# Performance work log

Hardware: AMD Instinct MI355X
Metric: run time of the kernel (lower is better)

Reference implementation:

```python
import jax, jax.numpy as jnp
import numpy as np

B, N, S, D, H = 32, 16384, 8, 64, 128  # batch, num_inputs, num_slots, slot_size(==input_size), mlp_hidden
ITERS = 3
EPS = 1e-8
LN_EPS = 1e-5


def _ln(x, g, b):
    m = jnp.mean(x, axis=-1, keepdims=True)
    v = jnp.mean((x - m) ** 2, axis=-1, keepdims=True)
    return (x - m) * jax.lax.rsqrt(v + LN_EPS) * g + b


def setup_inputs() -> dict:
    key = jax.random.key(0)
    ks = jax.random.split(key, 20)
    s = 0.02
    return {
        "x": jax.random.normal(ks[0], (B, N, D), jnp.float32),
        "slot_noise": jax.random.normal(ks[1], (B, S, D), jnp.float32),
        "slots_mu": jax.random.normal(ks[2], (1, S, D), jnp.float32),
        "slots_log_sigma": jax.random.normal(ks[3], (1, S, D), jnp.float32) * 0.1,
        "ln_in_g": jnp.ones((D,), jnp.float32), "ln_in_b": jnp.zeros((D,), jnp.float32),
        "ln_slot_g": jnp.ones((D,), jnp.float32), "ln_slot_b": jnp.zeros((D,), jnp.float32),
        "ln_mlp_g": jnp.ones((D,), jnp.float32), "ln_mlp_b": jnp.zeros((D,), jnp.float32),
        "Wq": jax.random.normal(ks[4], (D, D), jnp.float32) * s,
        "Wk": jax.random.normal(ks[5], (D, D), jnp.float32) * s,
        "Wv": jax.random.normal(ks[6], (D, D), jnp.float32) * s,
        "W_ih": jax.random.normal(ks[7], (3 * D, D), jnp.float32) * s,
        "W_hh": jax.random.normal(ks[8], (3 * D, D), jnp.float32) * s,
        "b_ih": jnp.zeros((3 * D,), jnp.float32),
        "b_hh": jnp.zeros((3 * D,), jnp.float32),
        "W1": jax.random.normal(ks[9], (H, D), jnp.float32) * s,
        "b1": jnp.zeros((H,), jnp.float32),
        "W2": jax.random.normal(ks[10], (D, H), jnp.float32) * s,
        "b2": jnp.zeros((D,), jnp.float32),
    }


def reference(x, slot_noise, slots_mu, slots_log_sigma,
              ln_in_g, ln_in_b, ln_slot_g, ln_slot_b, ln_mlp_g, ln_mlp_b,
              Wq, Wk, Wv, W_ih, W_hh, b_ih, b_hh, W1, b1, W2, b2):
    inputs = _ln(x, ln_in_g, ln_in_b)                      # [B,N,D]
    keys = inputs @ Wk.T                                   # [B,N,D]
    values = inputs @ Wv.T                                 # [B,N,D]
    slots = slots_mu + jnp.exp(slots_log_sigma) * slot_noise  # [B,S,D]
    scale = D ** (-0.5)
    for _ in range(ITERS):
        slots_prev = slots
        q = (_ln(slots, ln_slot_g, ln_slot_b) @ Wq.T) * scale   # [B,S,D]
        attn = jax.nn.softmax(jnp.einsum('bnd,bsd->bns', keys, q), axis=2) + EPS
        attn = attn / jnp.sum(attn, axis=1, keepdims=True)      # weighted mean over inputs
        updates = jnp.einsum('bns,bnd->bsd', attn, values)      # [B,S,D]
        # GRUCell(update, hidden=slots_prev), torch semantics
        gi = updates @ W_ih.T + b_ih
        gh = slots_prev @ W_hh.T + b_hh
        i_r, i_z, i_n = jnp.split(gi, 3, axis=-1)
        h_r, h_z, h_n = jnp.split(gh, 3, axis=-1)
        r = jax.nn.sigmoid(i_r + h_r)
        z = jax.nn.sigmoid(i_z + h_z)
        n = jnp.tanh(i_n + r * h_n)
        upd = (1.0 - z) * n + z * slots_prev
        # residual MLP (full_skip=False: residual around updates)
        slots = upd + jax.nn.relu(_ln(upd, ln_mlp_g, ln_mlp_b) @ W1.T + b1) @ W2.T + b2
    return slots
```

## Files before the change

### kernel.cpp

```cpp
#include <hip/hip_runtime.h>

#define BB 32
#define NN 16384

typedef __attribute__((ext_vector_type(4))) float f4;
typedef __attribute__((ext_vector_type(8))) short short8;

__device__ __forceinline__ unsigned int f2bf(float f) {
  unsigned int u = __float_as_uint(f);
  return (u + 0x7fffu + ((u >> 16) & 1u)) >> 16;
}
__device__ __forceinline__ short bfs(float f) { return (short)f2bf(f); }

__global__ void __launch_bounds__(256) prep_kernel(
    const float* __restrict__ Wq, const float* __restrict__ Wk,
    const float* __restrict__ W_ih, const float* __restrict__ Wv,
    float* __restrict__ M, float* __restrict__ Wihv)
{
  int id = blockIdx.x * 256 + threadIdx.x;
  if (id < 4096) {
    int e1 = id >> 6, e2 = id & 63;
    float acc = 0.f;
    for (int d = 0; d < 64; ++d) acc += Wq[d * 64 + e1] * Wk[d * 64 + e2];
    M[id] = acc;
  } else {
    int t = (id - 4096) >> 6, e = id & 63;
    float acc = 0.f;
    for (int k = 0; k < 64; ++k) acc += W_ih[t * 64 + k] * Wv[k * 64 + e];
    Wihv[t * 64 + e] = acc;
  }
}

__global__ void __launch_bounds__(64) init_qk_kernel(
    const float* __restrict__ noise, const float* __restrict__ mu,
    const float* __restrict__ lsig, float* __restrict__ slots,
    const float* __restrict__ gs, const float* __restrict__ bsl,
    const float* __restrict__ M, unsigned short* __restrict__ qkb)
{
  const int bsi = blockIdx.x, l = threadIdx.x;
  const int idx = bsi * 64 + l;
  __shared__ float sh[64];
  float v = mu[idx & 511] + __expf(lsig[idx & 511]) * noise[idx];
  slots[idx] = v;
  float sm = v, sq = v * v;
#pragma unroll
  for (int m = 1; m < 64; m <<= 1) { sm += __shfl_xor(sm, m); sq += __shfl_xor(sq, m); }
  float mean = sm * (1.f / 64.f);
  float var = sq * (1.f / 64.f) - mean * mean;
  sh[l] = (v - mean) * rsqrtf(var + 1e-5f) * gs[l] + bsl[l];
  float acc = 0.f;
  for (int k = 0; k < 64; ++k) acc += sh[k] * M[k * 64 + l];
  qkb[idx] = (unsigned short)f2bf(acc * 0.125f);
}

template <int MODE>
__global__ void __launch_bounds__(256) attn_kernel(
    const float* __restrict__ x, const unsigned short* __restrict__ Xin,
    const float* __restrict__ gin, const float* __restrict__ bin,
    unsigned short* __restrict__ Xout, unsigned short* __restrict__ XnT,
    const unsigned short* __restrict__ qkb,
    float* __restrict__ Wpart, float* __restrict__ cpart)
{
  constexpr int SMS = (MODE == 0) ? 16896 : 6720;
  __shared__ __align__(16) unsigned short SMEM[SMS];

  const int tid = threadIdx.x, wave = tid >> 6, lane = tid & 63;
  const int l15 = lane & 15, quad = lane >> 4;
  const int blk = blockIdx.x;
  const int b = blk >> 5;
  const int k0 = quad * 8;

  unsigned short* xt  = (MODE == 0) ? (SMEM + wave * 3584) : nullptr;
  unsigned short* Ptw = (MODE == 0) ? (SMEM + 14336 + wave * 640)
                                    : (SMEM + wave * 640);

  const unsigned short* qrow = qkb + (((b << 3) + (l15 & 7)) << 6) + k0;
  const short8 qkA0 = *(const short8*)qrow;
  const short8 qkA1 = *(const short8*)(qrow + 32);

  f4 g0a, g0b, g1a, g1b, h0a, h0b, h1a, h1b;
  if constexpr (MODE == 0) {
    g0a = *(const f4*)(gin + k0);      g0b = *(const f4*)(gin + k0 + 4);
    g1a = *(const f4*)(gin + k0 + 32); g1b = *(const f4*)(gin + k0 + 36);
    h0a = *(const f4*)(bin + k0);      h0b = *(const f4*)(bin + k0 + 4);
    h1a = *(const f4*)(bin + k0 + 32); h1b = *(const f4*)(bin + k0 + 36);
  }

  const size_t row00 = (size_t)blk * 512 + wave * 32 + l15;
  const int nt0 = ((blk & 31) << 4) + wave;

  f4 wacc[4];
#pragma unroll
  for (int t = 0; t < 4; ++t) wacc[t] = (f4){0.f, 0.f, 0.f, 0.f};
  float cac0 = 0.f, cac1 = 0.f, cac2 = 0.f, cac3 = 0.f;

  f4 cc[2][4];
  short8 aa[2][2];
  short8 cv[4];
  const unsigned short* vB =
      (MODE == 1) ? (XnT + ((((size_t)(b << 9)) + nt0) << 11) + (l15 << 5) + (quad << 3))
                  : nullptr;

  if constexpr (MODE == 0) {
    const float* xp = x + row00 * 64 + k0;
#pragma unroll
    for (int s = 0; s < 2; ++s) {
      const float* sp = xp + s * 1024;
      cc[s][0] = *(const f4*)sp;        cc[s][1] = *(const f4*)(sp + 4);
      cc[s][2] = *(const f4*)(sp + 32); cc[s][3] = *(const f4*)(sp + 36);
    }
  } else {
    const unsigned short* xb = Xin + row00 * 64 + k0;
#pragma unroll
    for (int s = 0; s < 2; ++s) {
      aa[s][0] = *(const short8*)(xb + s * 1024);
      aa[s][1] = *(const short8*)(xb + s * 1024 + 32);
    }
#pragma unroll
    for (int t = 0; t < 4; ++t)
      cv[t] = *(const short8*)(vB + (t << 9));
  }

#pragma unroll
  for (int u = 0; u < 4; ++u) {
    f4 nc[2][4];
    short8 na[2][2];
    short8 nv[4];
    if (u < 3) {
      if constexpr (MODE == 0) {
        const float* xp = x + (row00 + (size_t)(u + 1) * 128) * 64 + k0;
#pragma unroll
        for (int s = 0; s < 2; ++s) {
          const float* sp = xp + s * 1024;
          nc[s][0] = *(const f4*)sp;        nc[s][1] = *(const f4*)(sp + 4);
          nc[s][2] = *(const f4*)(sp + 32); nc[s][3] = *(const f4*)(sp + 36);
        }
      } else {
        const unsigned short* xb = Xin + (row00 + (size_t)(u + 1) * 128) * 64 + k0;
#pragma unroll
        for (int s = 0; s < 2; ++s) {
          na[s][0] = *(const short8*)(xb + s * 1024);
          na[s][1] = *(const short8*)(xb + s * 1024 + 32);
        }
#pragma unroll
        for (int t = 0; t < 4; ++t)
          nv[t] = *(const short8*)(vB + (t << 9) + ((size_t)(u + 1) << 13));
      }
    }

#pragma unroll
    for (int s = 0; s < 2; ++s) {
      short8 a0, a1;
      if constexpr (MODE == 0) {
        float sm = 0.f, sq = 0.f;
#pragma unroll
        for (int j = 0; j < 4; ++j) {
          float v0 = cc[s][0][j], v1 = cc[s][1][j], v2 = cc[s][2][j], v3 = cc[s][3][j];
          sm += v0 + v1 + v2 + v3;
          sq += v0 * v0 + v1 * v1 + v2 * v2 + v3 * v3;
        }
        sm += __shfl_xor(sm, 16); sq += __shfl_xor(sq, 16);
        sm += __shfl_xor(sm, 32); sq += __shfl_xor(sq, 32);
        const float mean = sm * (1.f / 64.f);
        const float var = sq * (1.f / 64.f) - mean * mean;
        const float rstd = rsqrtf(var + 1e-5f);
#pragma unroll
        for (int j = 0; j < 4; ++j) {
          a0[j]     = bfs((cc[s][0][j] - mean) * rstd * g0a[j] + h0a[j]);
          a0[j + 4] = bfs((cc[s][1][j] - mean) * rstd * g0b[j] + h0b[j]);
          a1[j]     = bfs((cc[s][2][j] - mean) * rstd * g1a[j] + h1a[j]);
          a1[j + 4] = bfs((cc[s][3][j] - mean) * rstd * g1b[j] + h1b[j]);
        }
        unsigned short* xo = Xout + (row00 + (size_t)u * 128 + s * 16) * 64 + k0;
        *(short8*)xo = a0;
        *(short8*)(xo + 32) = a1;
        const int nn = s * 16 + l15;
        unsigned short* xb0 = xt + (quad << 3) + nn;
#pragma unroll
        for (int jj = 0; jj < 8; ++jj) {
          xb0[(k0 + jj) * 56]      = (unsigned short)a0[jj];
          xb0[(k0 + jj + 32) * 56] = (unsigned short)a1[jj];
        }
      } else {
        a0 = aa[s][0]; a1 = aa[s][1];
      }

      f4 lg = (f4){0.f, 0.f, 0.f, 0.f};
      lg = __builtin_amdgcn_mfma_f32_16x16x32_bf16(qkA0, a0, lg, 0, 0, 0);
      lg = __builtin_amdgcn_mfma_f32_16x16x32_bf16(qkA1, a1, lg, 0, 0, 0);
      const float e0 = __expf(lg[0]), e1 = __expf(lg[1]);
      const float e2 = __expf(lg[2]), e3 = __expf(lg[3]);
      float ss = e0 + e1 + e2 + e3;
      ss += __shfl_xor(ss, 16);
      ss += __shfl_xor(ss, 32);
      const float rs = __builtin_amdgcn_rcpf(ss * 0.5f);
      const float p0 = e0 * rs, p1 = e1 * rs, p2 = e2 * rs, p3 = e3 * rs;
      cac0 += p0; cac1 += p1; cac2 += p2; cac3 += p3;
      unsigned short* pw = Ptw + (quad << 2) * 40 + s * 16 + l15;
      pw[0]   = (unsigned short)f2bf(p0);
      pw[40]  = (unsigned short)f2bf(p1);
      pw[80]  = (unsigned short)f2bf(p2);
      pw[120] = (unsigned short)f2bf(p3);
    }

    short8 pf = *(const short8*)(Ptw + l15 * 40 + quad * 8);
#pragma unroll
    for (int t = 0; t < 4; ++t) {
      short8 cvv;
      if constexpr (MODE == 0) {
        const int rr = t * 16 + l15;
        cvv = *(const short8*)(xt + rr * 56 + (((rr >> 3) & 3) << 3) + (quad << 3));
      } else {
        cvv = cv[t];
      }
      wacc[t] = __builtin_amdgcn_mfma_f32_16x16x32_bf16(pf, cvv, wacc[t], 0, 0, 0);
    }

    if constexpr (MODE == 0) {
      unsigned short* tb = XnT + ((((size_t)(b << 9)) + nt0 + (u << 2)) << 11);
#pragma unroll
      for (int pass = 0; pass < 4; ++pass) {
        const int e = (pass << 4) + (lane >> 2);
        const int no = (lane & 3) << 3;
        const short8 vv =
            *(const short8*)(xt + e * 56 + (((e >> 3) & 3) << 3) + no);
        *(short8*)(tb + (pass << 9) + ((lane >> 2) << 5) + no) = vv;
      }
    }

    if (u < 3) {
      if constexpr (MODE == 0) {
#pragma unroll
        for (int s = 0; s < 2; ++s)
#pragma unroll
          for (int j = 0; j < 4; ++j) cc[s][j] = nc[s][j];
      } else {
#pragma unroll
        for (int s = 0; s < 2; ++s) { aa[s][0] = na[s][0]; aa[s][1] = na[s][1]; }
#pragma unroll
        for (int t = 0; t < 4; ++t) cv[t] = nv[t];
      }
    }
  }

#pragma unroll
  for (int m = 1; m < 16; m <<= 1) {
    cac0 += __shfl_xor(cac0, m); cac1 += __shfl_xor(cac1, m);
    cac2 += __shfl_xor(cac2, m); cac3 += __shfl_xor(cac3, m);
  }
  float* redw;
  float* credw;
  if constexpr (MODE == 0) {
    redw  = (float*)(SMEM + wave * 3584);
    credw = (float*)(SMEM + wave * 3584 + 1024);
  } else {
    redw  = (float*)(SMEM + 2560) + wave * 512;
    credw = (float*)(SMEM + 6656) + wave * 8;
  }
  if (l15 == 0 && quad < 2) {
    credw[quad * 4 + 0] = cac0; credw[quad * 4 + 1] = cac1;
    credw[quad * 4 + 2] = cac2; credw[quad * 4 + 3] = cac3;
  }
  if (quad < 2) {
#pragma unroll
    for (int t = 0; t < 4; ++t)
#pragma unroll
      for (int r = 0; r < 4; ++r)
        redw[(quad * 4 + r) * 64 + (t << 4) + l15] = wacc[t][r];
  }
  __syncthreads();
  for (int i = tid; i < 512; i += 256) {
    float acc = 0.f;
#pragma unroll
    for (int w = 0; w < 4; ++w) {
      const float* rw = (MODE == 0) ? (const float*)(SMEM + w * 3584)
                                    : (const float*)(SMEM + 2560) + w * 512;
      acc += rw[i];
    }
    Wpart[(size_t)blk * 512 + i] = acc;
  }
  if (tid < 8) {
    float acc = 0.f;
#pragma unroll
    for (int w = 0; w < 4; ++w) {
      const float* cw = (MODE == 0) ? (const float*)(SMEM + w * 3584 + 1024)
                                    : (const float*)(SMEM + 6656) + w * 8;
      acc += cw[tid];
    }
    cpart[blk * 8 + tid] = acc;
  }
}

__global__ void __launch_bounds__(256) update_kernel(
    const float* __restrict__ Wpart, const float* __restrict__ cpart,
    const float* __restrict__ slots, float* __restrict__ out,
    const float* __restrict__ Wihv, const float* __restrict__ W_hh,
    const float* __restrict__ b_ih, const float* __restrict__ b_hh,
    const float* __restrict__ g_mlp, const float* __restrict__ b_mlp,
    const float* __restrict__ W1, const float* __restrict__ b1,
    const float* __restrict__ W2, const float* __restrict__ b2,
    const float* __restrict__ gs, const float* __restrict__ bsl,
    const float* __restrict__ M, unsigned short* __restrict__ qkb, int make_q)
{
  const int bs = blockIdx.x;
  const int b = bs >> 3, s = bs & 7;
  const int tid = threadIdx.x;
  const int l = tid & 63, cq = tid >> 6;
  __shared__ float wred[4][64];
  __shared__ float credS[4];
  __shared__ float u_sh[64], sp_sh[64], giA[192], ghA[192], uln_sh[64], h_sh[128];

  float wp = 0.f, cp2 = 0.f;
  for (int c = cq * 8; c < cq * 8 + 8; ++c) {
    wp += Wpart[(size_t)(((b << 5) + c) * 8 + s) * 64 + l];
    cp2 += cpart[((b << 5) + c) * 8 + s];
  }
  wred[cq][l] = wp;
  if (l == 0) credS[cq] = cp2;
  __syncthreads();

  float sp = 0.f;
  if (tid < 64) {
    const float cs = credS[0] + credS[1] + credS[2] + credS[3];
    const float u = (wred[0][l] + wred[1][l] + wred[2][l] + wred[3][l]) / cs;
    sp = slots[(b * 8 + s) * 64 + l];
    u_sh[l] = u; sp_sh[l] = sp;
  }
  __syncthreads();

  if (tid < 192) {
    float accI = b_ih[tid], accH = b_hh[tid];
    const float* wi = Wihv + tid * 64;
    const float* wh = W_hh + tid * 64;
    for (int k = 0; k < 64; ++k) { accI += u_sh[k] * wi[k]; accH += sp_sh[k] * wh[k]; }
    giA[tid] = accI; ghA[tid] = accH;
  }
  __syncthreads();

  float upd = 0.f;
  if (tid < 64) {
    const float rg = 1.f / (1.f + __expf(-(giA[l] + ghA[l])));
    const float zg = 1.f / (1.f + __expf(-(giA[64 + l] + ghA[64 + l])));
    const float ng = tanhf(giA[128 + l] + rg * ghA[128 + l]);
    upd = (1.f - zg) * ng + zg * sp;
    float sm = upd, sq = upd * upd;
#pragma unroll
    for (int m = 1; m < 64; m <<= 1) { sm += __shfl_xor(sm, m); sq += __shfl_xor(sq, m); }
    const float mean = sm * (1.f / 64.f);
    const float var = sq * (1.f / 64.f) - mean * mean;
    uln_sh[l] = (upd - mean) * rsqrtf(var + 1e-5f) * g_mlp[l] + b_mlp[l];
  }
  __syncthreads();

  if (tid < 128) {
    float acc = b1[tid];
    const float* w1 = W1 + tid * 64;
    for (int k = 0; k < 64; ++k) acc += uln_sh[k] * w1[k];
    h_sh[tid] = fmaxf(acc, 0.f);
  }
  __syncthreads();

  if (tid < 64) {
    float acc = b2[l];
    const float* w2 = W2 + l * 128;
    for (int k = 0; k < 128; ++k) acc += h_sh[k] * w2[k];
    const float sv = upd + acc;
    out[(b * 8 + s) * 64 + l] = sv;
    if (make_q) {
      float sm2 = sv, sq2 = sv * sv;
#pragma unroll
      for (int m = 1; m < 64; m <<= 1) { sm2 += __shfl_xor(sm2, m); sq2 += __shfl_xor(sq2, m); }
      const float mean2 = sm2 * (1.f / 64.f);
      const float var2 = sq2 * (1.f / 64.f) - mean2 * mean2;
      u_sh[l] = (sv - mean2) * rsqrtf(var2 + 1e-5f) * gs[l] + bsl[l];
      float qa = 0.f;
      for (int k = 0; k < 64; ++k) qa += u_sh[k] * M[k * 64 + l];
      qkb[(b * 8 + s) * 64 + l] = (unsigned short)f2bf(qa * 0.125f);
    }
  }
}

extern "C" void kernel_launch(void* const* d_in, const int* in_sizes, int n_in,
                              void* d_out, int out_size, void* d_ws, size_t ws_size,
                              hipStream_t stream) {
  const float* x       = (const float*)d_in[0];
  const float* noise   = (const float*)d_in[1];
  const float* mu      = (const float*)d_in[2];
  const float* lsig    = (const float*)d_in[3];
  const float* ln_in_g = (const float*)d_in[4];
  const float* ln_in_b = (const float*)d_in[5];
  const float* ln_sl_g = (const float*)d_in[6];
  const float* ln_sl_b = (const float*)d_in[7];
  const float* ln_ml_g = (const float*)d_in[8];
  const float* ln_ml_b = (const float*)d_in[9];
  const float* Wq      = (const float*)d_in[10];
  const float* Wk      = (const float*)d_in[11];
  const float* Wv      = (const float*)d_in[12];
  const float* W_ih    = (const float*)d_in[13];
  const float* W_hh    = (const float*)d_in[14];
  const float* b_ih    = (const float*)d_in[15];
  const float* b_hh    = (const float*)d_in[16];
  const float* W1      = (const float*)d_in[17];
  const float* b1      = (const float*)d_in[18];
  const float* W2      = (const float*)d_in[19];
  const float* b2      = (const float*)d_in[20];

  unsigned short* Xn  = (unsigned short*)d_ws;
  unsigned short* XnT = Xn + (size_t)BB * NN * 64;
  unsigned short* qkb = XnT + (size_t)BB * NN * 64;
  float* M     = (float*)(qkb + 16384);
  float* Wihv  = M + 4096;
  float* slots = Wihv + 12288;
  float* Wpart = slots + 16384;
  float* cpart = Wpart + (size_t)1024 * 512;

  prep_kernel<<<dim3(64), dim3(256), 0, stream>>>(Wq, Wk, W_ih, Wv, M, Wihv);
  init_qk_kernel<<<dim3(256), dim3(64), 0, stream>>>(
      noise, mu, lsig, slots, ln_sl_g, ln_sl_b, M, qkb);

  attn_kernel<0><<<dim3(1024), dim3(256), 0, stream>>>(
      x, nullptr, ln_in_g, ln_in_b, Xn, XnT, qkb, Wpart, cpart);

  for (int it = 0; it < 3; ++it) {
    update_kernel<<<dim3(256), dim3(256), 0, stream>>>(
        Wpart, cpart, slots, (it == 2) ? (float*)d_out : slots,
        Wihv, W_hh, b_ih, b_hh, ln_ml_g, ln_ml_b, W1, b1, W2, b2,
        ln_sl_g, ln_sl_b, M, qkb, (it < 2) ? 1 : 0);
    if (it < 2)
      attn_kernel<1><<<dim3(1024), dim3(256), 0, stream>>>(
          x, Xn, ln_in_g, ln_in_b, nullptr, XnT, qkb, Wpart, cpart);
  }
}
```

Measured before the change: 331.0 us.

## Store normalized inputs and transposed copy in FP8 and use FP8 MFMA in later iterations

The first attention pass now writes the layer-normed inputs and their transposed copy as FP8 instead of bf16. The two later attention passes read these FP8 buffers, quantize q·M and the attention probabilities to FP8, and use the fp8 MFMA instruction. This halves the global memory traffic of the bandwidth-bound re-reads of the 32x16384x64 input. The cost is lower precision in the logits and weighted sums, which may hurt accuracy against the reference tolerance.

New measurement: 298.5 us. 1.11x faster.

```diff
diff --git a/kernel.cpp b/kernel.cpp
--- a/kernel.cpp
+++ b/kernel.cpp
@@ -11,6 +11,12 @@
   return (u + 0x7fffu + ((u >> 16) & 1u)) >> 16;
 }
 __device__ __forceinline__ short bfs(float f) { return (short)f2bf(f); }
+
+__device__ __forceinline__ unsigned int pk4_fp8(float a, float b, float c, float d) {
+  int w = __builtin_amdgcn_cvt_pk_fp8_f32(a, b, 0, false);
+  w = __builtin_amdgcn_cvt_pk_fp8_f32(c, d, w, true);
+  return (unsigned int)w;
+}
 
 __global__ void __launch_bounds__(256) prep_kernel(
     const float* __restrict__ Wq, const float* __restrict__ Wk,
@@ -35,7 +41,7 @@
     const float* __restrict__ noise, const float* __restrict__ mu,
     const float* __restrict__ lsig, float* __restrict__ slots,
     const float* __restrict__ gs, const float* __restrict__ bsl,
-    const float* __restrict__ M, unsigned short* __restrict__ qkb)
+    const float* __restrict__ M, unsigned short* __restrict__ qkb16)
 {
   const int bsi = blockIdx.x, l = threadIdx.x;
   const int idx = bsi * 64 + l;
@@ -50,18 +56,18 @@
   sh[l] = (v - mean) * rsqrtf(var + 1e-5f) * gs[l] + bsl[l];
   float acc = 0.f;
   for (int k = 0; k < 64; ++k) acc += sh[k] * M[k * 64 + l];
-  qkb[idx] = (unsigned short)f2bf(acc * 0.125f);
+  qkb16[idx] = (unsigned short)f2bf(acc * 0.125f);
 }
 
 template <int MODE>
 __global__ void __launch_bounds__(256) attn_kernel(
-    const float* __restrict__ x, const unsigned short* __restrict__ Xin,
+    const float* __restrict__ x, const unsigned char* __restrict__ Xin,
     const float* __restrict__ gin, const float* __restrict__ bin,
-    unsigned short* __restrict__ Xout, unsigned short* __restrict__ XnT,
-    const unsigned short* __restrict__ qkb,
+    unsigned char* __restrict__ Xout, unsigned char* __restrict__ XnT,
+    const unsigned short* __restrict__ qkb16, const unsigned char* __restrict__ qkb8,
     float* __restrict__ Wpart, float* __restrict__ cpart)
 {
-  constexpr int SMS = (MODE == 0) ? 16896 : 6720;
+  constexpr int SMS = (MODE == 0) ? 16896 : 5440;
   __shared__ __align__(16) unsigned short SMEM[SMS];
 
   const int tid = threadIdx.x, wave = tid >> 6, lane = tid & 63;
@@ -71,12 +77,20 @@
   const int k0 = quad * 8;
 
   unsigned short* xt  = (MODE == 0) ? (SMEM + wave * 3584) : nullptr;
-  unsigned short* Ptw = (MODE == 0) ? (SMEM + 14336 + wave * 640)
-                                    : (SMEM + wave * 640);
-
-  const unsigned short* qrow = qkb + (((b << 3) + (l15 & 7)) << 6) + k0;
-  const short8 qkA0 = *(const short8*)qrow;
-  const short8 qkA1 = *(const short8*)(qrow + 32);
+  unsigned short* Pt16 = (MODE == 0) ? (SMEM + 14336 + wave * 640) : nullptr;
+  unsigned char*  Pt8  = (MODE == 1) ? ((unsigned char*)SMEM + wave * 640) : nullptr;
+
+  short8 qkA0_16, qkA1_16;
+  unsigned long qkA0_8 = 0, qkA1_8 = 0;
+  if constexpr (MODE == 0) {
+    const unsigned short* qrow = qkb16 + (((b << 3) + (l15 & 7)) << 6) + k0;
+    qkA0_16 = *(const short8*)qrow;
+    qkA1_16 = *(const short8*)(qrow + 32);
+  } else {
+    const unsigned char* qrow = qkb8 + (((b << 3) + (l15 & 7)) << 6) + k0;
+    qkA0_8 = *(const unsigned long*)qrow;
+    qkA1_8 = *(const unsigned long*)(qrow + 32);
+  }
 
   f4 g0a, g0b, g1a, g1b, h0a, h0b, h1a, h1b;
   if constexpr (MODE == 0) {
@@ -95,9 +109,9 @@
   float cac0 = 0.f, cac1 = 0.f, cac2 = 0.f, cac3 = 0.f;
 
   f4 cc[2][4];
-  short8 aa[2][2];
-  short8 cv[4];
-  const unsigned short* vB =
+  unsigned long a8[2][2];
+  unsigned long cv[4];
+  const unsigned char* vB =
       (MODE == 1) ? (XnT + ((((size_t)(b << 9)) + nt0) << 11) + (l15 << 5) + (quad << 3))
                   : nullptr;
 
@@ -110,22 +124,21 @@
       cc[s][2] = *(const f4*)(sp + 32); cc[s][3] = *(const f4*)(sp + 36);
     }
   } else {
-    const unsigned short* xb = Xin + row00 * 64 + k0;
+    const unsigned char* xb = Xin + row00 * 64 + k0;
 #pragma unroll
     for (int s = 0; s < 2; ++s) {
-      aa[s][0] = *(const short8*)(xb + s * 1024);
-      aa[s][1] = *(const short8*)(xb + s * 1024 + 32);
+      a8[s][0] = *(const unsigned long*)(xb + s * 1024);
+      a8[s][1] = *(const unsigned long*)(xb + s * 1024 + 32);
     }
 #pragma unroll
     for (int t = 0; t < 4; ++t)
-      cv[t] = *(const short8*)(vB + (t << 9));
+      cv[t] = *(const unsigned long*)(vB + (t << 9));
   }
 
 #pragma unroll
   for (int u = 0; u < 4; ++u) {
     f4 nc[2][4];
-    short8 na[2][2];
-    short8 nv[4];
+    unsigned long na[2][2], nv[4];
     if (u < 3) {
       if constexpr (MODE == 0) {
         const float* xp = x + (row00 + (size_t)(u + 1) * 128) * 64 + k0;
@@ -136,21 +149,22 @@
           nc[s][2] = *(const f4*)(sp + 32); nc[s][3] = *(const f4*)(sp + 36);
         }
       } else {
-        const unsigned short* xb = Xin + (row00 + (size_t)(u + 1) * 128) * 64 + k0;
+        const unsigned char* xb = Xin + (row00 + (size_t)(u + 1) * 128) * 64 + k0;
 #pragma unroll
         for (int s = 0; s < 2; ++s) {
-          na[s][0] = *(const short8*)(xb + s * 1024);
-          na[s][1] = *(const short8*)(xb + s * 1024 + 32);
+          na[s][0] = *(const unsigned long*)(xb + s * 1024);
+          na[s][1] = *(const unsigned long*)(xb + s * 1024 + 32);
         }
 #pragma unroll
         for (int t = 0; t < 4; ++t)
-          nv[t] = *(const short8*)(vB + (t << 9) + ((size_t)(u + 1) << 13));
+          nv[t] = *(const unsigned long*)(vB + (t << 9) + ((size_t)(u + 1) << 13));
       }
     }
 
 #pragma unroll
     for (int s = 0; s < 2; ++s) {
-      short8 a0, a1;
+      short8 a0_16, a1_16;
+      f4 lg = (f4){0.f, 0.f, 0.f, 0.f};
       if constexpr (MODE == 0) {
         float sm = 0.f, sq = 0.f;
 #pragma unroll
@@ -164,30 +178,39 @@
         const float mean = sm * (1.f / 64.f);
         const float var = sq * (1.f / 64.f) - mean * mean;
         const float rstd = rsqrtf(var + 1e-5f);
+        float f0[8], f1[8];
 #pragma unroll
         for (int j = 0; j < 4; ++j) {
-          a0[j]     = bfs((cc[s][0][j] - mean) * rstd * g0a[j] + h0a[j]);
-          a0[j + 4] = bfs((cc[s][1][j] - mean) * rstd * g0b[j] + h0b[j]);
-          a1[j]     = bfs((cc[s][2][j] - mean) * rstd * g1a[j] + h1a[j]);
-          a1[j + 4] = bfs((cc[s][3][j] - mean) * rstd * g1b[j] + h1b[j]);
+          f0[j]     = (cc[s][0][j] - mean) * rstd * g0a[j] + h0a[j];
+          f0[j + 4] = (cc[s][1][j] - mean) * rstd * g0b[j] + h0b[j];
+          f1[j]     = (cc[s][2][j] - mean) * rstd * g1a[j] + h1a[j];
+          f1[j + 4] = (cc[s][3][j] - mean) * rstd * g1b[j] + h1b[j];
         }
-        unsigned short* xo = Xout + (row00 + (size_t)u * 128 + s * 16) * 64 + k0;
-        *(short8*)xo = a0;
-        *(short8*)(xo + 32) = a1;
+#pragma unroll
+        for (int j = 0; j < 8; ++j) { a0_16[j] = bfs(f0[j]); a1_16[j] = bfs(f1[j]); }
+        unsigned char* xo = Xout + (row00 + (size_t)u * 128 + s * 16) * 64 + k0;
+        uint2 p0v2; p0v2.x = pk4_fp8(f0[0], f0[1], f0[2], f0[3]);
+        p0v2.y = pk4_fp8(f0[4], f0[5], f0[6], f0[7]);
+        *(uint2*)xo = p0v2;
+        uint2 p1v2; p1v2.x = pk4_fp8(f1[0], f1[1], f1[2], f1[3]);
+        p1v2.y = pk4_fp8(f1[4], f1[5], f1[6], f1[7]);
+        *(uint2*)(xo + 32) = p1v2;
         const int nn = s * 16 + l15;
         unsigned short* xb0 = xt + (quad << 3) + nn;
 #pragma unroll
         for (int jj = 0; jj < 8; ++jj) {
-          xb0[(k0 + jj) * 56]      = (unsigned short)a0[jj];
-          xb0[(k0 + jj + 32) * 56] = (unsigned short)a1[jj];
+          xb0[(k0 + jj) * 56]      = (unsigned short)a0_16[jj];
+          xb0[(k0 + jj + 32) * 56] = (unsigned short)a1_16[jj];
         }
+        lg = __builtin_amdgcn_mfma_f32_16x16x32_bf16(qkA0_16, a0_16, lg, 0, 0, 0);
+        lg = __builtin_amdgcn_mfma_f32_16x16x32_bf16(qkA1_16, a1_16, lg, 0, 0, 0);
       } else {
-        a0 = aa[s][0]; a1 = aa[s][1];
-      }
-
-      f4 lg = (f4){0.f, 0.f, 0.f, 0.f};
-      lg = __builtin_amdgcn_mfma_f32_16x16x32_bf16(qkA0, a0, lg, 0, 0, 0);
-      lg = __builtin_amdgcn_mfma_f32_16x16x32_bf16(qkA1, a1, lg, 0, 0, 0);
+        lg = __builtin_amdgcn_mfma_f32_16x16x32_fp8_fp8(
+            (long)qkA0_8, (long)a8[s][0], lg, 0, 0, 0);
+        lg = __builtin_amdgcn_mfma_f32_16x16x32_fp8_fp8(
+            (long)qkA1_8, (long)a8[s][1], lg, 0, 0, 0);
+      }
+
       const float e0 = __expf(lg[0]), e1 = __expf(lg[1]);
       const float e2 = __expf(lg[2]), e3 = __expf(lg[3]);
       float ss = e0 + e1 + e2 + e3;
@@ -196,36 +219,53 @@
       const float rs = __builtin_amdgcn_rcpf(ss * 0.5f);
       const float p0 = e0 * rs, p1 = e1 * rs, p2 = e2 * rs, p3 = e3 * rs;
       cac0 += p0; cac1 += p1; cac2 += p2; cac3 += p3;
-      unsigned short* pw = Ptw + (quad << 2) * 40 + s * 16 + l15;
-      pw[0]   = (unsigned short)f2bf(p0);
-      pw[40]  = (unsigned short)f2bf(p1);
-      pw[80]  = (unsigned short)f2bf(p2);
-      pw[120] = (unsigned short)f2bf(p3);
-    }
-
-    short8 pf = *(const short8*)(Ptw + l15 * 40 + quad * 8);
-#pragma unroll
-    for (int t = 0; t < 4; ++t) {
-      short8 cvv;
       if constexpr (MODE == 0) {
+        unsigned short* pw = Pt16 + (quad << 2) * 40 + s * 16 + l15;
+        pw[0]   = (unsigned short)f2bf(p0);
+        pw[40]  = (unsigned short)f2bf(p1);
+        pw[80]  = (unsigned short)f2bf(p2);
+        pw[120] = (unsigned short)f2bf(p3);
+      } else {
+        unsigned char* pw = Pt8 + (quad << 2) * 40 + s * 16 + l15;
+        const unsigned int w1 = (unsigned int)__builtin_amdgcn_cvt_pk_fp8_f32(p0, p1, 0, false);
+        const unsigned int w2 = (unsigned int)__builtin_amdgcn_cvt_pk_fp8_f32(p2, p3, 0, false);
+        pw[0]   = (unsigned char)(w1 & 0xff);
+        pw[40]  = (unsigned char)((w1 >> 8) & 0xff);
+        pw[80]  = (unsigned char)(w2 & 0xff);
+        pw[120] = (unsigned char)((w2 >> 8) & 0xff);
+      }
+    }
+
+    if constexpr (MODE == 0) {
+      short8 pf = *(const short8*)(Pt16 + l15 * 40 + quad * 8);
+#pragma unroll
+      for (int t = 0; t < 4; ++t) {
         const int rr = t * 16 + l15;
-        cvv = *(const short8*)(xt + rr * 56 + (((rr >> 3) & 3) << 3) + (quad << 3));
-      } else {
-        cvv = cv[t];
-      }
-      wacc[t] = __builtin_amdgcn_mfma_f32_16x16x32_bf16(pf, cvv, wacc[t], 0, 0, 0);
-    }
-
-    if constexpr (MODE == 0) {
-      unsigned short* tb = XnT + ((((size_t)(b << 9)) + nt0 + (u << 2)) << 11);
+        const short8 cvv =
+            *(const short8*)(xt + rr * 56 + (((rr >> 3) & 3) << 3) + (quad << 3));
+        wacc[t] = __builtin_amdgcn_mfma_f32_16x16x32_bf16(pf, cvv, wacc[t], 0, 0, 0);
+      }
+      unsigned char* tb = XnT + ((((size_t)(b << 9)) + nt0 + (u << 2)) << 11);
 #pragma unroll
       for (int pass = 0; pass < 4; ++pass) {
         const int e = (pass << 4) + (lane >> 2);
         const int no = (lane & 3) << 3;
         const short8 vv =
             *(const short8*)(xt + e * 56 + (((e >> 3) & 3) << 3) + no);
-        *(short8*)(tb + (pass << 9) + ((lane >> 2) << 5) + no) = vv;
-      }
+        float g[8];
+#pragma unroll
+        for (int j = 0; j < 8; ++j)
+          g[j] = __uint_as_float(((unsigned int)(unsigned short)vv[j]) << 16);
+        uint2 ov; ov.x = pk4_fp8(g[0], g[1], g[2], g[3]);
+        ov.y = pk4_fp8(g[4], g[5], g[6], g[7]);
+        *(uint2*)(tb + (e << 5) + no) = ov;
+      }
+    } else {
+      const unsigned long pf = *(const unsigned long*)(Pt8 + l15 * 40 + quad * 8);
+#pragma unroll
+      for (int t = 0; t < 4; ++t)
+        wacc[t] = __builtin_amdgcn_mfma_f32_16x16x32_fp8_fp8(
+            (long)pf, (long)cv[t], wacc[t], 0, 0, 0);
     }
 
     if (u < 3) {
@@ -236,7 +276,7 @@
           for (int j = 0; j < 4; ++j) cc[s][j] = nc[s][j];
       } else {
 #pragma unroll
-        for (int s = 0; s < 2; ++s) { aa[s][0] = na[s][0]; aa[s][1] = na[s][1]; }
+        for (int s = 0; s < 2; ++s) { a8[s][0] = na[s][0]; a8[s][1] = na[s][1]; }
 #pragma unroll
         for (int t = 0; t < 4; ++t) cv[t] = nv[t];
       }
@@ -254,8 +294,8 @@
     redw  = (float*)(SMEM + wave * 3584);
     credw = (float*)(SMEM + wave * 3584 + 1024);
   } else {
-    redw  = (float*)(SMEM + 2560) + wave * 512;
-    credw = (float*)(SMEM + 6656) + wave * 8;
+    redw  = (float*)(SMEM + 1280) + wave * 512;
+    credw = (float*)(SMEM + 5376) + wave * 8;
   }
   if (l15 == 0 && quad < 2) {
     credw[quad * 4 + 0] = cac0; credw[quad * 4 + 1] = cac1;
@@ -274,7 +314,7 @@
 #pragma unroll
     for (int w = 0; w < 4; ++w) {
       const float* rw = (MODE == 0) ? (const float*)(SMEM + w * 3584)
-                                    : (const float*)(SMEM + 2560) + w * 512;
+                                    : (const float*)(SMEM + 1280) + w * 512;
       acc += rw[i];
     }
     Wpart[(size_t)blk * 512 + i] = acc;
@@ -284,7 +324,7 @@
 #pragma unroll
     for (int w = 0; w < 4; ++w) {
       const float* cw = (MODE == 0) ? (const float*)(SMEM + w * 3584 + 1024)
-                                    : (const float*)(SMEM + 6656) + w * 8;
+                                    : (const float*)(SMEM + 5376) + w * 8;
       acc += cw[tid];
     }
     cpart[blk * 8 + tid] = acc;
@@ -300,7 +340,7 @@
     const float* __restrict__ W1, const float* __restrict__ b1,
     const float* __restrict__ W2, const float* __restrict__ b2,
     const float* __restrict__ gs, const float* __restrict__ bsl,
-    const float* __restrict__ M, unsigned short* __restrict__ qkb, int make_q)
+    const float* __restrict__ M, unsigned char* __restrict__ qkb8, int make_q)
 {
   const int bs = blockIdx.x;
   const int b = bs >> 3, s = bs & 7;
@@ -375,7 +415,9 @@
       u_sh[l] = (sv - mean2) * rsqrtf(var2 + 1e-5f) * gs[l] + bsl[l];
       float qa = 0.f;
       for (int k = 0; k < 64; ++k) qa += u_sh[k] * M[k * 64 + l];
-      qkb[(b * 8 + s) * 64 + l] = (unsigned short)f2bf(qa * 0.125f);
+      const unsigned int w =
+          (unsigned int)__builtin_amdgcn_cvt_pk_fp8_f32(qa * 0.125f, 0.f, 0, false);
+      qkb8[(b * 8 + s) * 64 + l] = (unsigned char)(w & 0xff);
     }
   }
 }
@@ -405,10 +447,11 @@
   const float* W2      = (const float*)d_in[19];
   const float* b2      = (const float*)d_in[20];
 
-  unsigned short* Xn  = (unsigned short*)d_ws;
-  unsigned short* XnT = Xn + (size_t)BB * NN * 64;
-  unsigned short* qkb = XnT + (size_t)BB * NN * 64;
-  float* M     = (float*)(qkb + 16384);
+  unsigned char* Xn8   = (unsigned char*)d_ws;
+  unsigned char* XnT8  = Xn8 + (size_t)BB * NN * 64;
+  unsigned short* qk16 = (unsigned short*)(XnT8 + (size_t)BB * NN * 64);
+  unsigned char* qk8   = (unsigned char*)(qk16 + 16384);
+  float* M     = (float*)(qk8 + 16384);
   float* Wihv  = M + 4096;
   float* slots = Wihv + 12288;
   float* Wpart = slots + 16384;
@@ -416,18 +459,18 @@
 
   prep_kernel<<<dim3(64), dim3(256), 0, stream>>>(Wq, Wk, W_ih, Wv, M, Wihv);
   init_qk_kernel<<<dim3(256), dim3(64), 0, stream>>>(
-      noise, mu, lsig, slots, ln_sl_g, ln_sl_b, M, qkb);
+      noise, mu, lsig, slots, ln_sl_g, ln_sl_b, M, qk16);
 
   attn_kernel<0><<<dim3(1024), dim3(256), 0, stream>>>(
-      x, nullptr, ln_in_g, ln_in_b, Xn, XnT, qkb, Wpart, cpart);
+      x, nullptr, ln_in_g, ln_in_b, Xn8, XnT8, qk16, nullptr, Wpart, cpart);
 
   for (int it = 0; it < 3; ++it) {
     update_kernel<<<dim3(256), dim3(256), 0, stream>>>(
         Wpart, cpart, slots, (it == 2) ? (float*)d_out : slots,
         Wihv, W_hh, b_ih, b_hh, ln_ml_g, ln_ml_b, W1, b1, W2, b2,
-        ln_sl_g, ln_sl_b, M, qkb, (it < 2) ? 1 : 0);
+        ln_sl_g, ln_sl_b, M, qk8, (it < 2) ? 1 : 0);
     if (it < 2)
       attn_kernel<1><<<dim3(1024), dim3(256), 0, stream>>>(
-          x, Xn, ln_in_g, ln_in_b, nullptr, XnT, qkb, Wpart, cpart);
-  }
-}
+          x, Xn8, ln_in_g, ln_in_b, nullptr, XnT8, nullptr, qk8, Wpart, cpart);
+  }
+}
```
